# Performance work log

Hardware: AMD Instinct MI355X
Metric: run time of the kernel (lower is better)

## Reference

```python
import jax, jax.numpy as jnp
import numpy as np

T, B, Y, H, R, L = 256, 1024, 32, 1024, 512, 2  # seq_len, batch, y_dim, h_dim, rnn_dim, n_layers


def setup_inputs() -> dict:
    key = jax.random.key(0)
    ks = jax.random.split(key, 18)
    s = jnp.float32(0.05)

    def w(k, shape):
        return jax.random.normal(k, shape, dtype=jnp.float32) * s

    return {
        "y": jax.random.normal(ks[0], (T, B, Y), dtype=jnp.float32),
        # decoder MLP: Linear(R->H), ReLU, Linear(H->H), ReLU
        "dec_w1": w(ks[1], (H, R)), "dec_b1": jnp.zeros((H,), jnp.float32),
        "dec_w2": w(ks[2], (H, H)), "dec_b2": jnp.zeros((H,), jnp.float32),
        # dec_mean: Linear(H->Y); dec_std: Linear(H->Y) + Softplus
        "mean_w": w(ks[3], (Y, H)), "mean_b": jnp.zeros((Y,), jnp.float32),
        "std_w": w(ks[4], (Y, H)), "std_b": jnp.zeros((Y,), jnp.float32),
        # 2-layer GRU, torch gate order (r, z, n)
        "gru_wih0": w(ks[5], (3 * R, Y)), "gru_whh0": w(ks[6], (3 * R, R)),
        "gru_bih0": jnp.zeros((3 * R,), jnp.float32), "gru_bhh0": jnp.zeros((3 * R,), jnp.float32),
        "gru_wih1": w(ks[7], (3 * R, R)), "gru_whh1": w(ks[8], (3 * R, R)),
        "gru_bih1": jnp.zeros((3 * R,), jnp.float32), "gru_bhh1": jnp.zeros((3 * R,), jnp.float32),
    }


def _gru_cell(x, h, wih, whh, bih, bhh):
    # torch GRUCell math, gates ordered (r, z, n)
    gi = x @ wih.T + bih          # [B, 3R]
    gh = h @ whh.T + bhh          # [B, 3R]
    ir, iz, inn = jnp.split(gi, 3, axis=-1)
    hr, hz, hn = jnp.split(gh, 3, axis=-1)
    r = jax.nn.sigmoid(ir + hr)
    z = jax.nn.sigmoid(iz + hz)
    n = jnp.tanh(inn + r * hn)
    return (1.0 - z) * n + z * h


def reference(y, dec_w1, dec_b1, dec_w2, dec_b2, mean_w, mean_b, std_w, std_b,
              gru_wih0, gru_whh0, gru_bih0, gru_bhh0,
              gru_wih1, gru_whh1, gru_bih1, gru_bhh1):
    log2pi = jnp.float32(np.log(2.0 * np.pi))
    batch = y.shape[1]
    h0 = jnp.zeros((L, batch, R), dtype=y.dtype)

    def step(carry, y_t):
        h, nll = carry
        # decode from top-layer hidden state (before the GRU update)
        d = jax.nn.relu(h[-1] @ dec_w1.T + dec_b1)
        d = jax.nn.relu(d @ dec_w2.T + dec_b2)
        mean_t = d @ mean_w.T + mean_b
        std_t = jax.nn.softplus(d @ std_w.T + std_b)
        # nll_gauss: 0.5 * sum((x-mu)^2/std^2 + 2*log(std) + log(2*pi))
        nll_t = 0.5 * jnp.sum((y_t - mean_t) ** 2 / (std_t ** 2)
                              + 2.0 * jnp.log(std_t) + log2pi)
        # single GRU step (2 layers)
        h_l0 = _gru_cell(y_t, h[0], gru_wih0, gru_whh0, gru_bih0, gru_bhh0)
        h_l1 = _gru_cell(h_l0, h[1], gru_wih1, gru_whh1, gru_bih1, gru_bhh1)
        return (jnp.stack([h_l0, h_l1]), nll + nll_t), None

    (_, nll), _ = jax.lax.scan(step, (h0, jnp.float32(0.0)), y)
    return nll
```

## Files before the change

### kernel.cpp

```cpp
#include <hip/hip_runtime.h>
#include <math.h>

#define TT   256
#define BB   1024
#define YDIM 32
#define HDIM 1024
#define RDIM 512

typedef __attribute__((ext_vector_type(8))) short frag8;
typedef __attribute__((ext_vector_type(4))) float f32x4;

#define LDS_BUF 16384

#define OFF_NLL   ((size_t)0)
#define OFF_HAF   ((size_t)4096)
#define SZ_HF     ((size_t)BB*RDIM*4)
#define OFF_HBF   (OFF_HAF + 2*SZ_HF)
#define OFF_HA16  (OFF_HBF + 2*SZ_HF)
#define SZ_H16    ((size_t)BB*RDIM*2)
#define OFF_HB16  (OFF_HA16 + 2*SZ_H16)
#define OFF_D1    (OFF_HB16 + 2*SZ_H16)
#define SZ_DBUF   ((size_t)BB*HDIM*2)
#define OFF_D2    (OFF_D1 + 2*SZ_DBUF)
#define OFF_Y16   (OFF_D2 + 2*SZ_DBUF)
#define OFF_WG0I  (OFF_Y16 + (size_t)TT*BB*YDIM*2)
#define OFF_WG0H  (OFF_WG0I + (size_t)1536*YDIM*2)
#define OFF_WG1I  (OFF_WG0H + (size_t)1536*RDIM*2)
#define OFF_WG1H  (OFF_WG1I + (size_t)1536*RDIM*2)
#define OFF_WD1   (OFF_WG1H + (size_t)1536*RDIM*2)
#define OFF_WD2   (OFF_WD1 + (size_t)HDIM*RDIM*2)
#define OFF_WMS   (OFF_WD2 + (size_t)HDIM*HDIM*2)
#define OFF_BI0   (OFF_WMS + (size_t)64*HDIM*2)
#define OFF_BH0   (OFF_BI0 + 1536*4)
#define OFF_BI1   (OFF_BH0 + 1536*4)
#define OFF_BH1   (OFF_BI1 + 1536*4)

__device__ __forceinline__ short f2bf(float f) {
  union { float f; unsigned u; } v; v.f = f;
  unsigned r = (v.u + 0x7fffu + ((v.u >> 16) & 1u)) >> 16;
  return (short)r;
}
__device__ __forceinline__ void cvt8(const float* s, short* d) {
  float4 a = *(const float4*)s;
  float4 b = *(const float4*)(s + 4);
  frag8 v;
  v[0]=f2bf(a.x); v[1]=f2bf(a.y); v[2]=f2bf(a.z); v[3]=f2bf(a.w);
  v[4]=f2bf(b.x); v[5]=f2bf(b.y); v[6]=f2bf(b.z); v[7]=f2bf(b.w);
  *(frag8*)d = v;
}
__device__ __forceinline__ int permRow(int n) {
  int q = n / 48, r = n - 48 * q, g = r >> 4, u = r & 15;
  return g * 512 + q * 16 + u;
}
__device__ __forceinline__ float sigf(float x) { return 1.0f / (1.0f + expf(-x)); }

__device__ __forceinline__ void gload16(const short* g, short* l) {
  __builtin_amdgcn_global_load_lds(
      (const __attribute__((address_space(1))) void*)g,
      (__attribute__((address_space(3))) void*)l, 16, 0, 0);
}

template<int N> __device__ __forceinline__ void waitv() {
  if constexpr (N == 0)      asm volatile("s_waitcnt vmcnt(0)" ::: "memory");
  else if constexpr (N == 6) asm volatile("s_waitcnt vmcnt(6)" ::: "memory");
  else if constexpr (N == 7) asm volatile("s_waitcnt vmcnt(7)" ::: "memory");
  else if constexpr (N == 8) asm volatile("s_waitcnt vmcnt(8)" ::: "memory");
  else                       asm volatile("s_waitcnt vmcnt(0)" ::: "memory");
}

template<int MF, int NF, int NROWSB>
__device__ __forceinline__ void kloop64(
    const short* __restrict__ A, int lda, int m0,
    const short* __restrict__ B, int ldb, int K,
    int wm, int wn, short* lds, f32x4 (*acc)[NF], int tid)
{
  const int l = tid & 63, w = tid >> 6, u = l & 15, quad = l >> 4;
  const int nk = K >> 6;
  constexpr int BUNITS = NROWSB << 3;
  constexpr int LPS = 4 + NROWSB / 32;

  auto stage = [&](int kc, int buf) {
    short* base = lds + buf * LDS_BUF;
    const int k0 = kc << 6;
    for (int c = (w << 6); c < 1024; c += 256) {
      int p = c + l, r = p >> 3, q = (p & 7) ^ (r & 7);
      gload16(A + (size_t)(m0 + r) * lda + k0 + (q << 3), base + (c << 3));
    }
    short* bb = base + 8192;
    for (int c = (w << 6); c < BUNITS; c += 256) {
      int p = c + l, r = p >> 3, q = (p & 7) ^ (r & 7);
      gload16(B + (size_t)r * ldb + k0 + (q << 3), bb + (c << 3));
    }
  };

  stage(0, 0);
  for (int kc = 0; kc < nk; ++kc) {
    asm volatile("s_waitcnt lgkmcnt(0)" ::: "memory");
    __builtin_amdgcn_s_barrier();
    if (kc + 1 < nk) {
      stage(kc + 1, (kc + 1) & 1);
      waitv<LPS>();
    } else {
      waitv<0>();
    }
    __builtin_amdgcn_s_barrier();
    asm volatile("" ::: "memory");
    const short* base = lds + (kc & 1) * LDS_BUF;
#pragma unroll
    for (int kk2 = 0; kk2 < 2; ++kk2) {
      const int q = (kk2 << 2) + quad;
      const int aoff = (q ^ (u & 7)) << 3;
      frag8 a[MF], b[NF];
#pragma unroll
      for (int i = 0; i < MF; ++i)
        a[i] = *(const frag8*)(base + ((wm + (i << 4) + u) << 6) + aoff);
#pragma unroll
      for (int f = 0; f < NF; ++f)
        b[f] = *(const frag8*)(base + 8192 + ((wn + (f << 4) + u) << 6) + aoff);
#pragma unroll
      for (int i = 0; i < MF; ++i)
#pragma unroll
        for (int f = 0; f < NF; ++f)
          acc[i][f] = __builtin_amdgcn_mfma_f32_16x16x32_bf16(a[i], b[f], acc[i][f], 0, 0, 0);
    }
  }
}

template<int MF, int NF>
__device__ __forceinline__ void kloop32(
    const short* __restrict__ A, int lda, int m0,
    const short* __restrict__ B, int nrowsB,
    int wm, int wn, short* lds, f32x4 (*acc)[NF], int tid)
{
  const int l = tid & 63, w = tid >> 6, u = l & 15, quad = l >> 4;
  short* base = lds;
  for (int c = (w << 6); c < 512; c += 256) {
    int p = c + l, r = p >> 2, q = (p & 3) ^ (r & 3);
    gload16(A + (size_t)(m0 + r) * lda + (q << 3), base + (c << 3));
  }
  short* bb = base + 4096;
  const int bunits = nrowsB << 2;
  for (int c = (w << 6); c < bunits; c += 256) {
    int p = c + l, r = p >> 2, q = (p & 3) ^ (r & 3);
    gload16(B + (size_t)r * 32 + (q << 3), bb + (c << 3));
  }
  __syncthreads();
  const int aoff = (quad ^ (u & 3)) << 3;
  frag8 a[MF], b[NF];
#pragma unroll
  for (int i = 0; i < MF; ++i)
    a[i] = *(const frag8*)(base + ((wm + (i << 4) + u) << 5) + aoff);
#pragma unroll
  for (int f = 0; f < NF; ++f)
    b[f] = *(const frag8*)(base + 4096 + ((wn + (f << 4) + u) << 5) + aoff);
#pragma unroll
  for (int i = 0; i < MF; ++i)
#pragma unroll
    for (int f = 0; f < NF; ++f)
      acc[i][f] = __builtin_amdgcn_mfma_f32_16x16x32_bf16(a[i], b[f], acc[i][f], 0, 0, 0);
  __syncthreads();
}

template<bool GI32>
__device__ void gru_tile(int mb, int nb,
                         const short* Ax, int ldx, const short* Wgi,
                         const short* Ah, const short* Wgh,
                         const float* bi, const float* bh,
                         const float* hold, float* hout, short* h16out,
                         short* lds, int tid)
{
  f32x4 zero = {0.f, 0.f, 0.f, 0.f};
  f32x4 gi[4][3], gh[4][3];
#pragma unroll
  for (int i = 0; i < 4; ++i)
#pragma unroll
    for (int f = 0; f < 3; ++f) { gi[i][f] = zero; gh[i][f] = zero; }
  const int w = tid >> 6, l = tid & 63, u = l & 15, quad = l >> 4;
  const int wm = (w & 1) * 64, wn = (w >> 1) * 48;
  if (GI32)
    kloop32<4, 3>(Ax, ldx, mb * 128, Wgi, 96, wm, wn, lds, gi, tid);
  else
    kloop64<4, 3, 96>(Ax, ldx, mb * 128, Wgi, RDIM, RDIM, wm, wn, lds, gi, tid);
  kloop64<4, 3, 96>(Ah, RDIM, mb * 128, Wgh, RDIM, RDIM, wm, wn, lds, gh, tid);

  const int np = nb * 96 + (w >> 1) * 48 + u;
  const float bir = bi[np], biz = bi[np + 16], bin = bi[np + 32];
  const float bhr = bh[np], bhz = bh[np + 16], bhn = bh[np + 32];
  const int unit = nb * 32 + (w >> 1) * 16 + u;
#pragma unroll
  for (int i = 0; i < 4; ++i)
#pragma unroll
    for (int j = 0; j < 4; ++j) {
      int row = mb * 128 + wm + 16 * i + quad * 4 + j;
      float r = sigf((gi[i][0][j] + bir) + (gh[i][0][j] + bhr));
      float z = sigf((gi[i][1][j] + biz) + (gh[i][1][j] + bhz));
      float n = tanhf((gi[i][2][j] + bin) + r * (gh[i][2][j] + bhn));
      float ho = hold[(size_t)row * RDIM + unit];
      float hn = (1.f - z) * n + z * ho;
      hout[(size_t)row * RDIM + unit] = hn;
      h16out[(size_t)row * RDIM + unit] = f2bf(hn);
    }
}

__device__ void dec_tile(int mb, int nb, const short* A, int lda, int K,
                         const short* W, const float* bias, short* outp,
                         short* lds, int tid)
{
  f32x4 zero = {0.f, 0.f, 0.f, 0.f};
  f32x4 acc[4][4];
#pragma unroll
  for (int i = 0; i < 4; ++i)
#pragma unroll
    for (int f = 0; f < 4; ++f) acc[i][f] = zero;
  const int w = tid >> 6, l = tid & 63, u = l & 15, quad = l >> 4;
  const int wm = (w & 1) * 64, wn = (w >> 1) * 64;
  kloop64<4, 4, 128>(A, lda, mb * 128, W, K, K, wm, wn, lds, acc, tid);
  const int colb = nb * 128 + wn + u;
  float bv[4];
#pragma unroll
  for (int f = 0; f < 4; ++f) bv[f] = bias[colb + 16 * f];
#pragma unroll
  for (int i = 0; i < 4; ++i)
#pragma unroll
    for (int f = 0; f < 4; ++f)
#pragma unroll
      for (int j = 0; j < 4; ++j) {
        int row = mb * 128 + wm + 16 * i + quad * 4 + j;
        float v = acc[i][f][j] + bv[f];
        if (v < 0.f) v = 0.f;
        outp[(size_t)row * HDIM + colb + 16 * f] = f2bf(v);
      }
}

__device__ void ms_tile(int mb, int tstep, const short* d2p, const short* Wms,
                        const float* mbias, const float* sbias, const float* y,
                        float* nll, short* lds, int tid)
{
  f32x4 zero = {0.f, 0.f, 0.f, 0.f};
  f32x4 acc[2][4];
#pragma unroll
  for (int i = 0; i < 2; ++i)
#pragma unroll
    for (int f = 0; f < 4; ++f) acc[i][f] = zero;
  const int w = tid >> 6, l = tid & 63, u = l & 15, quad = l >> 4;
  kloop64<2, 4, 64>(d2p, HDIM, mb * 128, Wms, HDIM, HDIM, w * 32, 0, lds, acc, tid);
  float lsum = 0.f;
#pragma unroll
  for (int i = 0; i < 2; ++i)
#pragma unroll
    for (int j = 0; j < 4; ++j) {
      int row = mb * 128 + w * 32 + 16 * i + quad * 4 + j;
      const float* yr = y + ((size_t)tstep * BB + row) * YDIM;
#pragma unroll
      for (int f = 0; f < 2; ++f) {
        int c = 16 * f + u;
        float m  = acc[i][f][j] + mbias[c];
        float sp = acc[i][f + 2][j] + sbias[c];
        float sg = (sp > 20.f) ? sp : log1pf(expf(sp));
        float dv = (yr[c] - m) / sg;
        lsum += dv * dv + 2.f * logf(sg) + 1.8378770664093453f;
      }
    }
  lsum *= 0.5f;
#pragma unroll
  for (int o = 32; o; o >>= 1) lsum += __shfl_xor(lsum, o);
  if (l == 0) atomicAdd(nll, lsum);
}

__global__ __launch_bounds__(256) void prepack_kernel(
    const float* y, const float* dw1, const float* dw2,
    const float* mw, const float* sw,
    const float* wih0, const float* whh0, const float* bih0, const float* bhh0,
    const float* wih1, const float* whh1, const float* bih1, const float* bhh1,
    char* __restrict__ ws)
{
  const size_t g = (size_t)blockIdx.x * 256 + threadIdx.x;
  const size_t N = (size_t)gridDim.x * 256;
  float4 z4 = {0.f, 0.f, 0.f, 0.f};
  float4* hz = (float4*)(ws + OFF_HAF);
  for (size_t i = g; i < (size_t)4 * BB * RDIM / 4; i += N) hz[i] = z4;
  int4 zi = {0, 0, 0, 0};
  int4* h16z = (int4*)(ws + OFF_HA16);
  for (size_t i = g; i < (size_t)4 * BB * RDIM / 8; i += N) h16z[i] = zi;
  if (g == 0) *(float*)(ws + OFF_NLL) = 0.f;

  short* y16  = (short*)(ws + OFF_Y16);
  short* Wg0i = (short*)(ws + OFF_WG0I);
  short* Wg0h = (short*)(ws + OFF_WG0H);
  short* Wg1i = (short*)(ws + OFF_WG1I);
  short* Wg1h = (short*)(ws + OFF_WG1H);
  short* Wd1  = (short*)(ws + OFF_WD1);
  short* Wd2  = (short*)(ws + OFF_WD2);
  short* Wms  = (short*)(ws + OFF_WMS);
  float* bi0  = (float*)(ws + OFF_BI0);
  float* bh0  = (float*)(ws + OFF_BH0);
  float* bi1  = (float*)(ws + OFF_BI1);
  float* bh1  = (float*)(ws + OFF_BH1);

  for (size_t s = g; s < (size_t)TT * BB * YDIM / 8; s += N)
    cvt8(y + s * 8, y16 + s * 8);
  for (size_t s = g; s < (size_t)1536 * RDIM / 8; s += N) {
    int row = (int)(s >> 6), seg = (int)(s & 63) << 3;
    int pr = permRow(row);
    cvt8(whh0 + (size_t)pr * RDIM + seg, Wg0h + (size_t)row * RDIM + seg);
    cvt8(wih1 + (size_t)pr * RDIM + seg, Wg1i + (size_t)row * RDIM + seg);
    cvt8(whh1 + (size_t)pr * RDIM + seg, Wg1h + (size_t)row * RDIM + seg);
  }
  for (size_t s = g; s < (size_t)1536 * YDIM / 8; s += N) {
    int row = (int)(s >> 2), seg = (int)(s & 3) << 3;
    cvt8(wih0 + (size_t)permRow(row) * YDIM + seg, Wg0i + (size_t)row * YDIM + seg);
  }
  for (size_t s = g; s < (size_t)HDIM * RDIM / 8; s += N)
    cvt8(dw1 + s * 8, Wd1 + s * 8);
  for (size_t s = g; s < (size_t)HDIM * HDIM / 8; s += N)
    cvt8(dw2 + s * 8, Wd2 + s * 8);
  for (size_t s = g; s < (size_t)64 * HDIM / 8; s += N) {
    int row = (int)(s >> 7), seg = (int)(s & 127) << 3;
    const float* src = (row < 32) ? (mw + (size_t)row * HDIM + seg)
                                  : (sw + (size_t)(row - 32) * HDIM + seg);
    cvt8(src, Wms + (size_t)row * HDIM + seg);
  }
  for (size_t s = g; s < 1536; s += N) {
    int pr = permRow((int)s);
    bi0[s] = bih0[pr]; bh0[s] = bhh0[pr];
    bi1[s] = bih1[pr]; bh1[s] = bhh1[pr];
  }
}

__global__ __launch_bounds__(256, 2) void phase_kernel(
    int p, const float* __restrict__ y,
    const float* db1, const float* db2, const float* mbias, const float* sbias,
    char* __restrict__ ws)
{
  __shared__ short lds[2 * LDS_BUF];
  const int tid = threadIdx.x;
  const int xcd = blockIdx.x & 7;
  const int s = blockIdx.x >> 3;
  const int cur = p & 1, prv = cur ^ 1;

  float* hAf = (float*)(ws + OFF_HAF);
  float* hBf = (float*)(ws + OFF_HBF);
  short* hA16 = (short*)(ws + OFF_HA16);
  short* hB16 = (short*)(ws + OFF_HB16);
  short* d10 = (short*)(ws + OFF_D1);
  short* d20 = (short*)(ws + OFF_D2);
  const short* y16 = (const short*)(ws + OFF_Y16);

  float* hAfc = hAf + (size_t)cur * BB * RDIM;
  float* hAfp = hAf + (size_t)prv * BB * RDIM;
  float* hBfc = hBf + (size_t)cur * BB * RDIM;
  float* hBfp = hBf + (size_t)prv * BB * RDIM;
  short* hA16c = hA16 + (size_t)cur * BB * RDIM;
  short* hA16p = hA16 + (size_t)prv * BB * RDIM;
  short* hB16c = hB16 + (size_t)cur * BB * RDIM;
  short* hB16p = hB16 + (size_t)prv * BB * RDIM;
  short* d1c = d10 + (size_t)cur * BB * HDIM;
  short* d1p = d10 + (size_t)prv * BB * HDIM;
  short* d2c = d20 + (size_t)cur * BB * HDIM;
  short* d2p = d20 + (size_t)prv * BB * HDIM;

  const short* Wg0i = (const short*)(ws + OFF_WG0I);
  const short* Wg0h = (const short*)(ws + OFF_WG0H);
  const short* Wg1i = (const short*)(ws + OFF_WG1I);
  const short* Wg1h = (const short*)(ws + OFF_WG1H);
  const short* Wd1  = (const short*)(ws + OFF_WD1);
  const short* Wd2  = (const short*)(ws + OFF_WD2);
  const short* Wms  = (const short*)(ws + OFF_WMS);
  const float* bi0  = (const float*)(ws + OFF_BI0);
  const float* bh0  = (const float*)(ws + OFF_BH0);
  const float* bi1  = (const float*)(ws + OFF_BI1);
  const float* bh1  = (const float*)(ws + OFF_BH1);
  float* nllp = (float*)(ws + OFF_NLL);

  if (s < 16) {
    if (p >= 1 && p <= 255) {
      int mb = 4 * (xcd & 1) + (s & 3);
      int nb = 4 * (xcd >> 1) + (s >> 2);
      gru_tile<false>(mb, nb,
                      hA16p, RDIM, Wg1i + (size_t)nb * 96 * RDIM,
                      hB16p, Wg1h + (size_t)nb * 96 * RDIM,
                      bi1, bh1, hBfp, hBfc, hB16c, lds, tid);
    }
  } else if (s < 32) {
    if (p <= 255) {
      int q = s - 16;
      int mb = 4 * (xcd & 1) + (q & 3);
      int nb = 4 * (xcd >> 1) + (q >> 2);
      gru_tile<true>(mb, nb,
                     y16 + (size_t)p * BB * YDIM, YDIM, Wg0i + (size_t)nb * 96 * YDIM,
                     hA16p, Wg0h + (size_t)nb * 96 * RDIM,
                     bi0, bh0, hAfp, hAfc, hA16c, lds, tid);
    }
  } else if (s < 40) {
    if (p >= 2 && p <= 257) {
      int q = s - 32;
      int mb = 4 * (xcd & 1) + (q & 3);
      int nb = 2 * (xcd >> 1) + (q >> 2);
      dec_tile(mb, nb, d1p, HDIM, HDIM, Wd2 + (size_t)nb * 128 * HDIM,
               db2, d2c, lds, tid);
    }
  } else if (s < 48) {
    if (p >= 1 && p <= 256) {
      int q = s - 40;
      int mb = 4 * (xcd & 1) + (q & 3);
      int nb = 2 * (xcd >> 1) + (q >> 2);
      dec_tile(mb, nb, hB16p, RDIM, RDIM, Wd1 + (size_t)nb * 128 * RDIM,
               db1, d1c, lds, tid);
    }
  } else {
    if (p >= 3 && p <= 258) {
      ms_tile(xcd, p - 3, d2p, Wms, mbias, sbias, y, nllp, lds, tid);
    }
  }
}

__global__ void finish_kernel(float* out, const char* ws)
{
  if (threadIdx.x == 0 && blockIdx.x == 0)
    out[0] = *(const float*)(ws + OFF_NLL);
}

extern "C" void kernel_launch(void* const* d_in, const int* in_sizes, int n_in,
                              void* d_out, int out_size, void* d_ws, size_t ws_size,
                              hipStream_t stream) {
  (void)in_sizes; (void)n_in; (void)out_size; (void)ws_size;
  const float* y    = (const float*)d_in[0];
  const float* dw1  = (const float*)d_in[1];
  const float* db1  = (const float*)d_in[2];
  const float* dw2  = (const float*)d_in[3];
  const float* db2  = (const float*)d_in[4];
  const float* mw   = (const float*)d_in[5];
  const float* mbias= (const float*)d_in[6];
  const float* sw   = (const float*)d_in[7];
  const float* sbias= (const float*)d_in[8];
  const float* wih0 = (const float*)d_in[9];
  const float* whh0 = (const float*)d_in[10];
  const float* bih0 = (const float*)d_in[11];
  const float* bhh0 = (const float*)d_in[12];
  const float* wih1 = (const float*)d_in[13];
  const float* whh1 = (const float*)d_in[14];
  const float* bih1 = (const float*)d_in[15];
  const float* bhh1 = (const float*)d_in[16];
  char* ws = (char*)d_ws;
  float* out = (float*)d_out;

  prepack_kernel<<<256, 256, 0, stream>>>(y, dw1, dw2, mw, sw,
                                          wih0, whh0, bih0, bhh0,
                                          wih1, whh1, bih1, bhh1, ws);
  for (int p = 0; p < 259; ++p)
    phase_kernel<<<392, 256, 0, stream>>>(p, y, db1, db2, mbias, sbias, ws);
  finish_kernel<<<1, 1, 0, stream>>>(out, ws);
}
```

Measured before the change: 5.370 ms.

## Load GEMM weight fragments directly from global memory in pre-packed layout

The weight (B) operand of every MFMA GEMM is no longer staged through LDS. Instead, the one-time conversion pass repacks each weight matrix into a per-k-chunk, fragment-ordered bf16 layout, and each wave reads its B fragments straight into registers with vector global loads. This halves the LDS buffer, since it now holds only the A tile, and removes the LDS write/read round trip and related traffic for weights. In exchange, B loads go to L2/global on each k-iteration without a deep prefetch, so their latency may be exposed. Waves that share a column slice also read the same data redundantly, and more VGPRs are held for the b[2][NF] fragments.

```diff
diff --git a/kernel.cpp b/kernel.cpp
--- a/kernel.cpp
+++ b/kernel.cpp
@@ -10,7 +10,7 @@
 typedef __attribute__((ext_vector_type(8))) short frag8;
 typedef __attribute__((ext_vector_type(4))) float f32x4;
 
-#define LDS_BUF 16384
+#define LDS_BUF 8192
 
 #define OFF_NLL   ((size_t)0)
 #define OFF_HAF   ((size_t)4096)
@@ -62,44 +62,44 @@
 
 template<int N> __device__ __forceinline__ void waitv() {
   if constexpr (N == 0)      asm volatile("s_waitcnt vmcnt(0)" ::: "memory");
-  else if constexpr (N == 6) asm volatile("s_waitcnt vmcnt(6)" ::: "memory");
-  else if constexpr (N == 7) asm volatile("s_waitcnt vmcnt(7)" ::: "memory");
-  else if constexpr (N == 8) asm volatile("s_waitcnt vmcnt(8)" ::: "memory");
+  else if constexpr (N == 4) asm volatile("s_waitcnt vmcnt(4)" ::: "memory");
   else                       asm volatile("s_waitcnt vmcnt(0)" ::: "memory");
 }
 
 template<int MF, int NF, int NROWSB>
 __device__ __forceinline__ void kloop64(
     const short* __restrict__ A, int lda, int m0,
-    const short* __restrict__ B, int ldb, int K,
+    const short* __restrict__ B, int K,
     int wm, int wn, short* lds, f32x4 (*acc)[NF], int tid)
 {
   const int l = tid & 63, w = tid >> 6, u = l & 15, quad = l >> 4;
   const int nk = K >> 6;
-  constexpr int BUNITS = NROWSB << 3;
-  constexpr int LPS = 4 + NROWSB / 32;
-
-  auto stage = [&](int kc, int buf) {
+
+  auto stageA = [&](int kc, int buf) {
     short* base = lds + buf * LDS_BUF;
     const int k0 = kc << 6;
     for (int c = (w << 6); c < 1024; c += 256) {
       int p = c + l, r = p >> 3, q = (p & 7) ^ (r & 7);
       gload16(A + (size_t)(m0 + r) * lda + k0 + (q << 3), base + (c << 3));
     }
-    short* bb = base + 8192;
-    for (int c = (w << 6); c < BUNITS; c += 256) {
-      int p = c + l, r = p >> 3, q = (p & 7) ^ (r & 7);
-      gload16(B + (size_t)r * ldb + k0 + (q << 3), bb + (c << 3));
-    }
   };
 
-  stage(0, 0);
+  const short* Bl = B + ((size_t)quad * NROWSB + wn + u) * 8;
+
+  stageA(0, 0);
   for (int kc = 0; kc < nk; ++kc) {
     asm volatile("s_waitcnt lgkmcnt(0)" ::: "memory");
     __builtin_amdgcn_s_barrier();
+    frag8 b[2][NF];
+    const short* Bkc = Bl + (size_t)kc * NROWSB * 64;
+#pragma unroll
+    for (int kk2 = 0; kk2 < 2; ++kk2)
+#pragma unroll
+      for (int f = 0; f < NF; ++f)
+        b[kk2][f] = *(const frag8*)(Bkc + ((size_t)kk2 * 4 * NROWSB + f * 16) * 8);
     if (kc + 1 < nk) {
-      stage(kc + 1, (kc + 1) & 1);
-      waitv<LPS>();
+      stageA(kc + 1, (kc + 1) & 1);
+      waitv<4>();
     } else {
       waitv<0>();
     }
@@ -110,18 +110,15 @@
     for (int kk2 = 0; kk2 < 2; ++kk2) {
       const int q = (kk2 << 2) + quad;
       const int aoff = (q ^ (u & 7)) << 3;
-      frag8 a[MF], b[NF];
+      frag8 a[MF];
 #pragma unroll
       for (int i = 0; i < MF; ++i)
         a[i] = *(const frag8*)(base + ((wm + (i << 4) + u) << 6) + aoff);
 #pragma unroll
-      for (int f = 0; f < NF; ++f)
-        b[f] = *(const frag8*)(base + 8192 + ((wn + (f << 4) + u) << 6) + aoff);
-#pragma unroll
       for (int i = 0; i < MF; ++i)
 #pragma unroll
         for (int f = 0; f < NF; ++f)
-          acc[i][f] = __builtin_amdgcn_mfma_f32_16x16x32_bf16(a[i], b[f], acc[i][f], 0, 0, 0);
+          acc[i][f] = __builtin_amdgcn_mfma_f32_16x16x32_bf16(a[i], b[kk2][f], acc[i][f], 0, 0, 0);
     }
   }
 }
@@ -129,7 +126,7 @@
 template<int MF, int NF>
 __device__ __forceinline__ void kloop32(
     const short* __restrict__ A, int lda, int m0,
-    const short* __restrict__ B, int nrowsB,
+    const short* __restrict__ B,
     int wm, int wn, short* lds, f32x4 (*acc)[NF], int tid)
 {
   const int l = tid & 63, w = tid >> 6, u = l & 15, quad = l >> 4;
@@ -138,21 +135,17 @@
     int p = c + l, r = p >> 2, q = (p & 3) ^ (r & 3);
     gload16(A + (size_t)(m0 + r) * lda + (q << 3), base + (c << 3));
   }
-  short* bb = base + 4096;
-  const int bunits = nrowsB << 2;
-  for (int c = (w << 6); c < bunits; c += 256) {
-    int p = c + l, r = p >> 2, q = (p & 3) ^ (r & 3);
-    gload16(B + (size_t)r * 32 + (q << 3), bb + (c << 3));
-  }
+  frag8 b[NF];
+  const short* Bl = B + ((size_t)quad * 96 + wn + u) * 8;
+#pragma unroll
+  for (int f = 0; f < NF; ++f)
+    b[f] = *(const frag8*)(Bl + f * 128);
   __syncthreads();
   const int aoff = (quad ^ (u & 3)) << 3;
-  frag8 a[MF], b[NF];
+  frag8 a[MF];
 #pragma unroll
   for (int i = 0; i < MF; ++i)
     a[i] = *(const frag8*)(base + ((wm + (i << 4) + u) << 5) + aoff);
-#pragma unroll
-  for (int f = 0; f < NF; ++f)
-    b[f] = *(const frag8*)(base + 4096 + ((wn + (f << 4) + u) << 5) + aoff);
 #pragma unroll
   for (int i = 0; i < MF; ++i)
 #pragma unroll
@@ -178,10 +171,10 @@
   const int w = tid >> 6, l = tid & 63, u = l & 15, quad = l >> 4;
   const int wm = (w & 1) * 64, wn = (w >> 1) * 48;
   if (GI32)
-    kloop32<4, 3>(Ax, ldx, mb * 128, Wgi, 96, wm, wn, lds, gi, tid);
+    kloop32<4, 3>(Ax, ldx, mb * 128, Wgi, wm, wn, lds, gi, tid);
   else
-    kloop64<4, 3, 96>(Ax, ldx, mb * 128, Wgi, RDIM, RDIM, wm, wn, lds, gi, tid);
-  kloop64<4, 3, 96>(Ah, RDIM, mb * 128, Wgh, RDIM, RDIM, wm, wn, lds, gh, tid);
+    kloop64<4, 3, 96>(Ax, ldx, mb * 128, Wgi, RDIM, wm, wn, lds, gi, tid);
+  kloop64<4, 3, 96>(Ah, RDIM, mb * 128, Wgh, RDIM, wm, wn, lds, gh, tid);
 
   const int np = nb * 96 + (w >> 1) * 48 + u;
   const float bir = bi[np], biz = bi[np + 16], bin = bi[np + 32];
@@ -214,7 +207,7 @@
     for (int f = 0; f < 4; ++f) acc[i][f] = zero;
   const int w = tid >> 6, l = tid & 63, u = l & 15, quad = l >> 4;
   const int wm = (w & 1) * 64, wn = (w >> 1) * 64;
-  kloop64<4, 4, 128>(A, lda, mb * 128, W, K, K, wm, wn, lds, acc, tid);
+  kloop64<4, 4, 128>(A, lda, mb * 128, W, K, wm, wn, lds, acc, tid);
   const int colb = nb * 128 + wn + u;
   float bv[4];
 #pragma unroll
@@ -243,7 +236,7 @@
 #pragma unroll
     for (int f = 0; f < 4; ++f) acc[i][f] = zero;
   const int w = tid >> 6, l = tid & 63, u = l & 15, quad = l >> 4;
-  kloop64<2, 4, 64>(d2p, HDIM, mb * 128, Wms, HDIM, HDIM, w * 32, 0, lds, acc, tid);
+  kloop64<2, 4, 64>(d2p, HDIM, mb * 128, Wms, HDIM, w * 32, 0, lds, acc, tid);
   float lsum = 0.f;
 #pragma unroll
   for (int i = 0; i < 2; ++i)
@@ -299,26 +292,40 @@
 
   for (size_t s = g; s < (size_t)TT * BB * YDIM / 8; s += N)
     cvt8(y + s * 8, y16 + s * 8);
-  for (size_t s = g; s < (size_t)1536 * RDIM / 8; s += N) {
-    int row = (int)(s >> 6), seg = (int)(s & 63) << 3;
-    int pr = permRow(row);
-    cvt8(whh0 + (size_t)pr * RDIM + seg, Wg0h + (size_t)row * RDIM + seg);
-    cvt8(wih1 + (size_t)pr * RDIM + seg, Wg1i + (size_t)row * RDIM + seg);
-    cvt8(whh1 + (size_t)pr * RDIM + seg, Wg1h + (size_t)row * RDIM + seg);
-  }
-  for (size_t s = g; s < (size_t)1536 * YDIM / 8; s += N) {
-    int row = (int)(s >> 2), seg = (int)(s & 3) << 3;
-    cvt8(wih0 + (size_t)permRow(row) * YDIM + seg, Wg0i + (size_t)row * YDIM + seg);
-  }
-  for (size_t s = g; s < (size_t)HDIM * RDIM / 8; s += N)
-    cvt8(dw1 + s * 8, Wd1 + s * 8);
-  for (size_t s = g; s < (size_t)HDIM * HDIM / 8; s += N)
-    cvt8(dw2 + s * 8, Wd2 + s * 8);
-  for (size_t s = g; s < (size_t)64 * HDIM / 8; s += N) {
-    int row = (int)(s >> 7), seg = (int)(s & 127) << 3;
-    const float* src = (row < 32) ? (mw + (size_t)row * HDIM + seg)
-                                  : (sw + (size_t)(row - 32) * HDIM + seg);
-    cvt8(src, Wms + (size_t)row * HDIM + seg);
+
+  for (size_t s = g; s < 98304; s += N) {
+    int blk = (int)(s / 6144), wv = (int)(s % 6144);
+    int kcq = wv / 96, rl = wv % 96;
+    int col = (kcq >> 3) * 64 + (kcq & 7) * 8;
+    int pr = permRow(blk * 96 + rl);
+    cvt8(whh0 + (size_t)pr * RDIM + col, Wg0h + s * 8);
+    cvt8(wih1 + (size_t)pr * RDIM + col, Wg1i + s * 8);
+    cvt8(whh1 + (size_t)pr * RDIM + col, Wg1h + s * 8);
+  }
+  for (size_t s = g; s < 6144; s += N) {
+    int blk = (int)(s / 384), wv = (int)(s % 384);
+    int q = wv / 96, rl = wv % 96;
+    int pr = permRow(blk * 96 + rl);
+    cvt8(wih0 + (size_t)pr * YDIM + q * 8, Wg0i + s * 8);
+  }
+  for (size_t s = g; s < 65536; s += N) {
+    int blk = (int)(s >> 13), wv = (int)(s & 8191);
+    int kcq = wv >> 7, rl = wv & 127;
+    int col = (kcq >> 3) * 64 + (kcq & 7) * 8;
+    cvt8(dw1 + (size_t)(blk * 128 + rl) * RDIM + col, Wd1 + s * 8);
+  }
+  for (size_t s = g; s < 131072; s += N) {
+    int blk = (int)(s >> 14), wv = (int)(s & 16383);
+    int kcq = wv >> 7, rl = wv & 127;
+    int col = (kcq >> 3) * 64 + (kcq & 7) * 8;
+    cvt8(dw2 + (size_t)(blk * 128 + rl) * HDIM + col, Wd2 + s * 8);
+  }
+  for (size_t s = g; s < 8192; s += N) {
+    int kcq = (int)(s >> 6), rl = (int)(s & 63);
+    int col = (kcq >> 3) * 64 + (kcq & 7) * 8;
+    const float* src = (rl < 32) ? (mw + (size_t)rl * HDIM + col)
+                                 : (sw + (size_t)(rl - 32) * HDIM + col);
+    cvt8(src, Wms + s * 8);
   }
   for (size_t s = g; s < 1536; s += N) {
     int pr = permRow((int)s);
```

Result: slower. 6.547 ms (+21.9%).
